# Kernel tuning notes

Hardware: AMD Instinct MI355X
Metric: run time of the kernel (lower is better)

## Reference

```python
import jax, jax.numpy as jnp
import numpy as np

B, C, T = 16, 256, 1024
KERNEL_SPECS = [(3, 6), (5, 6), (9, 6)]
D = sum(o for _, o in KERNEL_SPECS)  # 18
TAU = 5.0
ALPHA = float(np.exp(-1.0 / TAU))
THRESHOLD = 0.01


def _dwconv(x, w, b, k):
    # x: (B,C,T), w: (C*out_per, 1, k) depthwise grouped conv, 'same' padding
    pad = (k - 1) // 2
    out = jax.lax.conv_general_dilated(
        x, w, window_strides=(1,), padding=[(pad, pad)],
        dimension_numbers=('NCH', 'OIH', 'NCH'), feature_group_count=C)
    return out + b[None, :, None]


def setup_inputs() -> dict:
    key = jax.random.key(0)
    ks = jax.random.split(key, 12)
    x = jax.random.normal(ks[0], (B, C, T), dtype=jnp.float32)
    params = {}
    for i, (k, op) in enumerate(KERNEL_SPECS):
        fan = k  # depthwise: 1 input channel per group
        bound = 1.0 / np.sqrt(fan)
        params[f'w{k}'] = jax.random.uniform(ks[1 + 2 * i], (C * op, 1, k), minval=-bound, maxval=bound, dtype=jnp.float32)
        params[f'b{k}'] = jax.random.uniform(ks[2 + 2 * i], (C * op,), minval=-bound, maxval=bound, dtype=jnp.float32)
    bound = 1.0 / np.sqrt(D)
    reduce_w = jax.random.uniform(ks[7], (C, D), minval=-bound, maxval=bound, dtype=jnp.float32)
    reduce_b = jax.random.uniform(ks[8], (C,), minval=-bound, maxval=bound, dtype=jnp.float32)
    latency_scale = jnp.asarray(5.0, dtype=jnp.float32)
    # xavier_uniform then zero diagonal
    g = np.sqrt(6.0 / (C + C))
    output_gates = jax.random.uniform(ks[9], (C, C), minval=-g, maxval=g, dtype=jnp.float32)
    output_gates = output_gates * (1.0 - jnp.eye(C, dtype=jnp.float32))
    filter_weights = 0.01 * jax.random.normal(ks[10], (C, C, D), dtype=jnp.float32)
    return dict(x=x, w3=params['w3'], b3=params['b3'], w5=params['w5'], b5=params['b5'],
                w9=params['w9'], b9=params['b9'], reduce_w=reduce_w, reduce_b=reduce_b,
                latency_scale=latency_scale, output_gates=output_gates,
                filter_weights=filter_weights)


def _lif_latency(drive):
    # drive: (B,C,T) -> latency (B,C); value T means 'no spike'
    Bc, Cc, Tc = drive.shape
    V0 = jnp.zeros((Bc, Cc), dtype=drive.dtype)
    fired0 = jnp.zeros((Bc, Cc), dtype=bool)
    lat0 = jnp.full((Bc, Cc), float(Tc), dtype=drive.dtype)

    def step(carry, inp):
        V, fired, lat = carry
        t, d_t = inp
        V = ALPHA * V + (1.0 - ALPHA) * d_t
        just = (V >= THRESHOLD) & (~fired)
        lat = jnp.where(just, t.astype(lat.dtype), lat)
        return (V, fired | just, lat), None

    ts = jnp.arange(Tc, dtype=jnp.float32)
    (_, _, lat), _ = jax.lax.scan(step, (V0, fired0, lat0), (ts, jnp.moveaxis(drive, 2, 0)))
    return lat


def reference(x, w3, b3, w5, b5, w9, b9, reduce_w, reduce_b,
              latency_scale, output_gates, filter_weights):
    ws = {3: (w3, b3), 5: (w5, b5), 9: (w9, b9)}
    outs = []
    for k, op in KERNEL_SPECS:
        w, b = ws[k]
        o = _dwconv(x, w, b, k)              # (B, C*op, T)
        outs.append(o.reshape(B, C, op, T))
    dendritic_drive = jnp.concatenate(outs, axis=2)  # (B, C, D, T)
    # grouped 1x1 reduce conv == per-channel weighted sum over D
    drive = jnp.einsum('bcdt,cd->bct', dendritic_drive, reduce_w) + reduce_b[None, :, None]
    true_lat = _lif_latency(drive)                    # (B, C)
    scale = jnp.maximum(latency_scale, 0.001)
    act = jnp.exp(-true_lat / scale)                  # (B, C)
    # padded kernel database (C, D, T)
    kp = jnp.zeros((C, D, T), dtype=x.dtype)
    off = 0
    for k, op in KERNEL_SPECS:
        w, _ = ws[k]
        kp = kp.at[:, off:off + op, :k].set(w.reshape(C, op, k))
        off += op
    coeff_base = output_gates[:, :, None] * filter_weights  # (Cj, Cc, D)
    recon = jnp.einsum('jcd,bc,cdt->bjt', coeff_base, act, kp)  # (B, C, T)
    return recon, x, true_lat, act
```

## Files before the change

### kernel.cpp

```cpp
#include <hip/hip_runtime.h>
#include <math.h>

#define Bb 16
#define Cc 256
#define Tt 1024

#define OFF_X   4194304
#define OFF_LAT 8388608
#define OFF_ACT 8392704

#define ALPHA_F 0.8187307530779818f
#define BETA_F  0.18126924692201815f
#define A16_F   0.04076220397836621f
#define THR_F   0.01f

__global__ __launch_bounds__(256) void k_prep(
    const float* __restrict__ w3, const float* __restrict__ b3,
    const float* __restrict__ w5, const float* __restrict__ b5,
    const float* __restrict__ w9, const float* __restrict__ b9,
    const float* __restrict__ rw, const float* __restrict__ rb,
    const float* __restrict__ og, const float* __restrict__ fw,
    float* __restrict__ effb,
    float* __restrict__ H)
{
    const int c = threadIdx.x;
    const int j = blockIdx.x;
    if (j < 256) {
        float h[9];
        #pragma unroll
        for (int t = 0; t < 9; ++t) h[t] = 0.f;
        const float g = og[j * 256 + c];
        const float* fwp = fw + (j * 256 + c) * 18;
        const float* w3p = w3 + c * 18;
        const float* w5p = w5 + c * 30;
        const float* w9p = w9 + c * 54;
        #pragma unroll
        for (int oi = 0; oi < 6; ++oi) {
            const float f3 = fwp[oi], f5 = fwp[6 + oi], f9 = fwp[12 + oi];
            #pragma unroll
            for (int t = 0; t < 3; ++t) h[t] = fmaf(f3, w3p[oi * 3 + t], h[t]);
            #pragma unroll
            for (int t = 0; t < 5; ++t) h[t] = fmaf(f5, w5p[oi * 5 + t], h[t]);
            #pragma unroll
            for (int t = 0; t < 9; ++t) h[t] = fmaf(f9, w9p[oi * 9 + t], h[t]);
        }
        #pragma unroll
        for (int t = 0; t < 9; ++t) H[(j * 9 + t) * 256 + c] = g * h[t];
    } else {
        float e[9];
        #pragma unroll
        for (int r = 0; r < 9; ++r) e[r] = 0.f;
        const float* rwp = rw + c * 18;
        const float* w3p = w3 + c * 18;
        const float* w5p = w5 + c * 30;
        const float* w9p = w9 + c * 54;
        float be = rb[c];
        #pragma unroll
        for (int oi = 0; oi < 6; ++oi) {
            const float r3 = rwp[oi], r5 = rwp[6 + oi], r9 = rwp[12 + oi];
            #pragma unroll
            for (int i = 0; i < 3; ++i) e[3 + i] = fmaf(r3, w3p[oi * 3 + i], e[3 + i]);
            #pragma unroll
            for (int i = 0; i < 5; ++i) e[2 + i] = fmaf(r5, w5p[oi * 5 + i], e[2 + i]);
            #pragma unroll
            for (int i = 0; i < 9; ++i) e[i]     = fmaf(r9, w9p[oi * 9 + i], e[i]);
            be = fmaf(r3, b3[c * 6 + oi], be);
            be = fmaf(r5, b5[c * 6 + oi], be);
            be = fmaf(r9, b9[c * 6 + oi], be);
        }
        #pragma unroll
        for (int r = 0; r < 9; ++r) effb[c * 10 + r] = e[r];
        effb[c * 10 + 9] = be;
    }
}

__global__ __launch_bounds__(256) void k_lif(
    const float* __restrict__ x, const float* __restrict__ effb,
    const float* __restrict__ ls, float* __restrict__ out)
{
    const int lane = threadIdx.x & 63;
    const int wid  = threadIdx.x >> 6;
    const int row  = blockIdx.x * 4 + wid;
    const int c    = row & 255;

    const float* xrow  = x + (size_t)row * Tt;
    const float4* xrow4 = reinterpret_cast<const float4*>(xrow);

    const int s = lane * 16;
    float xr[24];
    #pragma unroll
    for (int q = 0; q < 6; ++q) {
        const int t0 = s - 4 + 4 * q;
        float4 v = make_float4(0.f, 0.f, 0.f, 0.f);
        if (t0 >= 0 && t0 < Tt) v = xrow4[t0 >> 2];
        xr[q * 4 + 0] = v.x; xr[q * 4 + 1] = v.y;
        xr[q * 4 + 2] = v.z; xr[q * 4 + 3] = v.w;
    }

    float e[9];
    const float* ep = effb + c * 10;
    #pragma unroll
    for (int r = 0; r < 9; ++r) e[r] = ep[r];
    const float be = ep[9];

    float d[16];
    #pragma unroll
    for (int i = 0; i < 16; ++i) {
        float acc = be;
        #pragma unroll
        for (int r = 0; r < 9; ++r) acc = fmaf(e[r], xr[i + r], acc);
        d[i] = acc;
    }

    float Bl = 0.f;
    #pragma unroll
    for (int i = 0; i < 16; ++i) Bl = fmaf(ALPHA_F, Bl, BETA_F * d[i]);

    float Av = A16_F, Bv = Bl;
    #pragma unroll
    for (int o = 1; o < 64; o <<= 1) {
        const float Ap = __shfl_up(Av, (unsigned)o);
        const float Bp = __shfl_up(Bv, (unsigned)o);
        if (lane >= o) { Bv = fmaf(Av, Bp, Bv); Av = Av * Ap; }
    }
    float Vin = __shfl_up(Bv, 1u);
    if (lane == 0) Vin = 0.f;

    int local = -1;
    float V = Vin;
    #pragma unroll
    for (int i = 0; i < 16; ++i) {
        V = fmaf(ALPHA_F, V, BETA_F * d[i]);
        if (local < 0 && V >= THR_F) local = i;
    }
    const unsigned long long m = __ballot(local >= 0);
    float latf = 1024.f;
    if (m) {
        const int fl = __ffsll((unsigned long long)m) - 1;
        const int li = __shfl(local, fl);
        latf = (float)(fl * 16 + li);
    }
    const float scale = fmaxf(ls[0], 0.001f);
    const float act = expf(-latf / scale);

    float4* ox4 = reinterpret_cast<float4*>(out + OFF_X) + (size_t)row * 256;
    #pragma unroll
    for (int q = 0; q < 4; ++q) ox4[lane + 64 * q] = xrow4[lane + 64 * q];

    if (lane == 0) {
        out[OFF_LAT + row] = latf;
        out[OFF_ACT + row] = act;
    }
}

__global__ __launch_bounds__(256) void k_recon(
    const float* __restrict__ H, const float* __restrict__ actp,
    float* __restrict__ out)
{
    const int tid = threadIdx.x;
    const int bid = blockIdx.x;
    const int b = bid >> 8, j = bid & 255;

    const float a = actp[b * 256 + tid];
    float p[9];
    #pragma unroll
    for (int t = 0; t < 9; ++t) p[t] = a * H[(j * 9 + t) * 256 + tid];

    #pragma unroll
    for (int t = 0; t < 9; ++t) {
        #pragma unroll
        for (int o = 32; o > 0; o >>= 1) p[t] += __shfl_xor(p[t], o);
    }

    __shared__ float red[4][12];
    __shared__ float rs[12];
    const int lane = tid & 63, wid = tid >> 6;
    if (lane == 0) {
        #pragma unroll
        for (int t = 0; t < 9; ++t) red[wid][t] = p[t];
    }
    __syncthreads();
    if (tid < 9) rs[tid] = red[0][tid] + red[1][tid] + red[2][tid] + red[3][tid];
    __syncthreads();

    float4 v = make_float4(0.f, 0.f, 0.f, 0.f);
    if (tid == 0)      v = make_float4(rs[0], rs[1], rs[2], rs[3]);
    else if (tid == 1) v = make_float4(rs[4], rs[5], rs[6], rs[7]);
    else if (tid == 2) v = make_float4(rs[8], 0.f, 0.f, 0.f);
    reinterpret_cast<float4*>(out)[(size_t)bid * 256 + tid] = v;
}

extern "C" void kernel_launch(void* const* d_in, const int* in_sizes, int n_in,
                              void* d_out, int out_size, void* d_ws, size_t ws_size,
                              hipStream_t stream) {
    const float* x  = (const float*)d_in[0];
    const float* w3 = (const float*)d_in[1];
    const float* b3 = (const float*)d_in[2];
    const float* w5 = (const float*)d_in[3];
    const float* b5 = (const float*)d_in[4];
    const float* w9 = (const float*)d_in[5];
    const float* b9 = (const float*)d_in[6];
    const float* rw = (const float*)d_in[7];
    const float* rb = (const float*)d_in[8];
    const float* ls = (const float*)d_in[9];
    const float* og = (const float*)d_in[10];
    const float* fw = (const float*)d_in[11];
    float* out = (float*)d_out;

    float* effb = (float*)d_ws;
    float* H    = (float*)d_ws + 2560;

    k_prep<<<dim3(257), dim3(256), 0, stream>>>(w3, b3, w5, b5, w9, b9,
                                                rw, rb, og, fw, effb, H);
    k_lif<<<dim3(1024), dim3(256), 0, stream>>>(x, effb, ls, out);
    k_recon<<<dim3(4096), dim3(256), 0, stream>>>(H, out + OFF_ACT, out);
}
```

Measured before the change: 120.1 us.

## Fuse prep and LIF kernels, compute effective conv weights per wave

Merges the weight-prep kernel and the LIF kernel into one launch: blocks beyond 1024 build the H reconstruction table, and LIF blocks compute their per-channel collapsed 9-tap filter and bias in-wave using an 18-lane product followed by a butterfly shuffle reduction. This removes one kernel launch and the dependency on an effb workspace round trip. In exchange, each of the 4096 rows redundantly recomputes its channel's effective filter, adding shuffle work per wave.

```diff
diff --git a/kernel.cpp b/kernel.cpp
--- a/kernel.cpp
+++ b/kernel.cpp
@@ -14,18 +14,22 @@
 #define A16_F   0.04076220397836621f
 #define THR_F   0.01f
 
-__global__ __launch_bounds__(256) void k_prep(
+__global__ __launch_bounds__(256) void k_main(
+    const float* __restrict__ x,
     const float* __restrict__ w3, const float* __restrict__ b3,
     const float* __restrict__ w5, const float* __restrict__ b5,
     const float* __restrict__ w9, const float* __restrict__ b9,
     const float* __restrict__ rw, const float* __restrict__ rb,
-    const float* __restrict__ og, const float* __restrict__ fw,
-    float* __restrict__ effb,
-    float* __restrict__ H)
+    const float* __restrict__ ls, const float* __restrict__ og,
+    const float* __restrict__ fw,
+    float* __restrict__ H, float* __restrict__ out)
 {
-    const int c = threadIdx.x;
-    const int j = blockIdx.x;
-    if (j < 256) {
+    const int bid = blockIdx.x;
+    const int tid = threadIdx.x;
+
+    if (bid >= 1024) {
+        const int j = bid - 1024;
+        const int c = tid;
         float h[9];
         #pragma unroll
         for (int t = 0; t < 9; ++t) h[t] = 0.f;
@@ -46,42 +50,47 @@
         }
         #pragma unroll
         for (int t = 0; t < 9; ++t) H[(j * 9 + t) * 256 + c] = g * h[t];
-    } else {
-        float e[9];
-        #pragma unroll
-        for (int r = 0; r < 9; ++r) e[r] = 0.f;
-        const float* rwp = rw + c * 18;
-        const float* w3p = w3 + c * 18;
-        const float* w5p = w5 + c * 30;
-        const float* w9p = w9 + c * 54;
-        float be = rb[c];
-        #pragma unroll
-        for (int oi = 0; oi < 6; ++oi) {
-            const float r3 = rwp[oi], r5 = rwp[6 + oi], r9 = rwp[12 + oi];
-            #pragma unroll
-            for (int i = 0; i < 3; ++i) e[3 + i] = fmaf(r3, w3p[oi * 3 + i], e[3 + i]);
-            #pragma unroll
-            for (int i = 0; i < 5; ++i) e[2 + i] = fmaf(r5, w5p[oi * 5 + i], e[2 + i]);
-            #pragma unroll
-            for (int i = 0; i < 9; ++i) e[i]     = fmaf(r9, w9p[oi * 9 + i], e[i]);
-            be = fmaf(r3, b3[c * 6 + oi], be);
-            be = fmaf(r5, b5[c * 6 + oi], be);
-            be = fmaf(r9, b9[c * 6 + oi], be);
+        return;
+    }
+
+    const int lane = tid & 63;
+    const int wid  = tid >> 6;
+    const int row  = bid * 4 + wid;
+    const int c    = row & 255;
+
+    float el[9];
+    #pragma unroll
+    for (int r = 0; r < 9; ++r) el[r] = 0.f;
+    float bl = 0.f;
+    if (lane < 18) {
+        const float r = rw[c * 18 + lane];
+        if (lane < 6) {
+            const int oi = lane;
+            #pragma unroll
+            for (int i = 0; i < 3; ++i) el[3 + i] = r * w3[c * 18 + oi * 3 + i];
+            bl = r * b3[c * 6 + oi];
+        } else if (lane < 12) {
+            const int oi = lane - 6;
+            #pragma unroll
+            for (int i = 0; i < 5; ++i) el[2 + i] = r * w5[c * 30 + oi * 5 + i];
+            bl = r * b5[c * 6 + oi];
+        } else {
+            const int oi = lane - 12;
+            #pragma unroll
+            for (int i = 0; i < 9; ++i) el[i] = r * w9[c * 54 + oi * 9 + i];
+            bl = r * b9[c * 6 + oi];
         }
-        #pragma unroll
-        for (int r = 0; r < 9; ++r) effb[c * 10 + r] = e[r];
-        effb[c * 10 + 9] = be;
-    }
-}
-
-__global__ __launch_bounds__(256) void k_lif(
-    const float* __restrict__ x, const float* __restrict__ effb,
-    const float* __restrict__ ls, float* __restrict__ out)
-{
-    const int lane = threadIdx.x & 63;
-    const int wid  = threadIdx.x >> 6;
-    const int row  = blockIdx.x * 4 + wid;
-    const int c    = row & 255;
+    }
+    #pragma unroll
+    for (int o = 1; o < 64; o <<= 1) {
+        #pragma unroll
+        for (int r = 0; r < 9; ++r) el[r] += __shfl_xor(el[r], o);
+        bl += __shfl_xor(bl, o);
+    }
+    float e[9];
+    #pragma unroll
+    for (int r = 0; r < 9; ++r) e[r] = el[r];
+    const float be = bl + rb[c];
 
     const float* xrow  = x + (size_t)row * Tt;
     const float4* xrow4 = reinterpret_cast<const float4*>(xrow);
@@ -96,12 +105,6 @@
         xr[q * 4 + 0] = v.x; xr[q * 4 + 1] = v.y;
         xr[q * 4 + 2] = v.z; xr[q * 4 + 3] = v.w;
     }
-
-    float e[9];
-    const float* ep = effb + c * 10;
-    #pragma unroll
-    for (int r = 0; r < 9; ++r) e[r] = ep[r];
-    const float be = ep[9];
 
     float d[16];
     #pragma unroll
@@ -207,11 +210,9 @@
     const float* fw = (const float*)d_in[11];
     float* out = (float*)d_out;
 
-    float* effb = (float*)d_ws;
-    float* H    = (float*)d_ws + 2560;
-
-    k_prep<<<dim3(257), dim3(256), 0, stream>>>(w3, b3, w5, b5, w9, b9,
-                                                rw, rb, og, fw, effb, H);
-    k_lif<<<dim3(1024), dim3(256), 0, stream>>>(x, effb, ls, out);
+    float* H = (float*)d_ws;
+
+    k_main<<<dim3(1280), dim3(256), 0, stream>>>(x, w3, b3, w5, b5, w9, b9,
+                                                 rw, rb, ls, og, fw, H, out);
     k_recon<<<dim3(4096), dim3(256), 0, stream>>>(H, out + OFF_ACT, out);
 }
```

Result: faster. 113.2 us (median of 2 runs) (-5.7%).
